# Kernel optimization log

Measured on AMD Instinct MI355X. Metric: run time of the kernel, lower is better.

The kernel has to match this reference:

```python
import jax, jax.numpy as jnp
import numpy as np
from jax import lax

TH = 1.0  # fire threshold (init kwarg th)


def setup_inputs() -> dict:
    key = jax.random.key(0)
    k0, k1, k2 = jax.random.split(key, 3)
    B, T, C = 32, 3000, 512
    hs_pad = jax.random.normal(k0, (B, T, C), dtype=jnp.float32)
    hs_mask = jnp.ones((B, 1, T), dtype=jnp.int32)  # espnet-style [B,1,T] mask, 1=valid
    # Conv1d(C, C, k=5) weight layout [out, in, k], fan-in scaled
    conv_w = jax.random.normal(k1, (C, C, 5), dtype=jnp.float32) * (1.0 / np.sqrt(C * 5))
    conv_b = jnp.zeros((C,), dtype=jnp.float32)
    # Linear(C, 1): stored transposed as [C, 1]
    lin_w = jax.random.normal(k2, (C, 1), dtype=jnp.float32) * (1.0 / np.sqrt(C))
    lin_b = jnp.zeros((1,), dtype=jnp.float32)
    return dict(hs_pad=hs_pad, hs_mask=hs_mask, conv_w=conv_w, conv_b=conv_b,
                lin_w=lin_w, lin_b=lin_b)


def _cif_single(alpha, h, th):
    """Integrate-and-fire for one sequence. alpha:[T], h:[T,C] -> [T,C] (zero padded)."""
    T, C = h.shape

    def step(carry, inp):
        acc, hacc = carry
        a, hu = inp
        acc2 = acc + a
        fired = acc2 >= th
        a1 = th - acc  # = th - (acc2 - a)
        emit = jnp.where(fired, hacc + a1 * hu, jnp.zeros_like(hu))
        new_acc = jnp.where(fired, a - a1, acc2)
        new_h = jnp.where(fired, (a - a1) * hu, hacc + a * hu)
        return (new_acc, new_h), (fired, emit)

    (acc_f, h_f), (fired, emits) = lax.scan(
        step, (jnp.float32(0.0), jnp.zeros((C,), h.dtype)), (alpha, h))
    nfire = jnp.cumsum(fired.astype(jnp.int32))
    idx = jnp.where(fired, nfire - 1, T)  # non-fired steps dump into scratch row T
    out = jnp.zeros((T + 1, C), h.dtype).at[idx].add(emits)
    # tail emission: remaining mass >= th/2
    tail = acc_f >= th * 0.5
    tail_idx = jnp.where(tail, nfire[-1], T)
    out = out.at[tail_idx].add(jnp.where(tail, h_f, jnp.zeros_like(h_f)))
    return out[:T]  # fires <= T always (alpha < 1 = th)


def _forward(hs_pad, hs_mask, conv_w, conv_b, lin_w, lin_b):
    B, T, C = hs_pad.shape
    # Conv1d(C,C,5,pad=2) on [B,C,T]  (note: self.norm is never used in the torch forward)
    x = lax.conv_general_dilated(hs_pad.transpose(0, 2, 1), conv_w, (1,), [(2, 2)],
                                 dimension_numbers=('NCH', 'OIH', 'NCH'))
    x = jax.nn.relu(x + conv_b[None, :, None])  # [B,C,T]
    alpha = jax.nn.sigmoid(jnp.einsum('bct,co->bto', x, lin_w) + lin_b)  # [B,T,1]
    # ys_pad=None -> T_y = 0; loss computed BEFORE masking (as in torch)
    loss_pen = jnp.abs(alpha.sum(axis=1) - 0.0).sum()
    a = alpha[..., 0] * (hs_mask[:, 0, :] != 0).astype(alpha.dtype)  # masked_fill(mask==0, 0)
    cs = jax.vmap(lambda av, hv: _cif_single(av, hv, TH))(a, hs_pad)  # [B,T,C]
    cs_mask = jnp.any(cs != 0.0, axis=-1)[:, None, :]  # [B,1,T]
    return cs, cs_mask, loss_pen


def reference(hs_pad, hs_mask, conv_w, conv_b, lin_w, lin_b):
    return _forward(hs_pad, hs_mask, conv_w, conv_b, lin_w, lin_b)
```

## Files before the change

### kernel.cpp

```cpp
#include <hip/hip_runtime.h>
#include <math.h>

#define B_ 32
#define T_ 3000
#define C_ 512
#define THf 1.0f
#define KW 2560

typedef _Float16 f16;
typedef _Float16 half8 __attribute__((ext_vector_type(8)));
typedef float floatx4 __attribute__((ext_vector_type(4)));

#define GLOBAL_AS __attribute__((address_space(1)))
#define LDS_AS __attribute__((address_space(3)))

#define WHI_OFF   0
#define WLO_OFF   2621440
#define PL_OFF    5242880
#define ALPHA_OFF 8314880
#define SEGI_OFF  8698880
#define SEGW_OFF  9466880
#define TOT_OFF   10234880

#define CS_SIZE  ((size_t)B_ * T_ * C_)
#define MASK_OFF CS_SIZE
#define LOSS_OFF (CS_SIZE + (size_t)B_ * T_)

__global__ __launch_bounds__(256) void w_prep_kernel(
    const float* __restrict__ W, f16* __restrict__ whi, f16* __restrict__ wlo)
{
    int idx = blockIdx.x * 256 + threadIdx.x;
    if (idx >= 512 * KW) return;
    int ie = idx & 7;
    int o  = (idx >> 3) & 511;
    int i8 = (idx >> 12) & 63;
    int k  = idx >> 18;
    int i  = i8 * 8 + ie;
    float w = W[o * KW + i * 5 + k];
    f16 h = (f16)w;
    whi[idx] = h;
    wlo[idx] = (f16)((w - (float)h) * 2048.0f);
}

#define A_ROWS 132
#define ALO_OFF_E  8448
#define WB_OFF_E   16896
#define WB_ARR_E   4096

__global__ __launch_bounds__(256, 2) void conv_alpha_mfma(
    const float* __restrict__ hs, const f16* __restrict__ whi_g,
    const f16* __restrict__ wlo_g, const float* __restrict__ conv_b,
    const float* __restrict__ lin_w, float* __restrict__ pl)
{
    __shared__ f16 sm[33280];
    f16* Ahi = sm;
    f16* Alo = sm + ALO_OFF_E;
    f16* Wb  = sm + WB_OFF_E;

    int tid = threadIdx.x;
    int bid = blockIdx.x;
    int nb  = bid & 3;
    int mtg = bid >> 2;
    int b   = mtg / 24;
    int mt  = mtg - b * 24;
    int t0  = mt * 128;

    int wid = tid >> 6, l = tid & 63;
    int wm = wid >> 1, wn = wid & 1;
    int l15 = l & 15, l4 = l >> 4;

    const float* hb = hs + (size_t)b * T_ * C_;
    int o0 = nb * 128;

    floatx4 acc1[4][4], acc2[4][4];
#pragma unroll
    for (int mf = 0; mf < 4; ++mf)
#pragma unroll
        for (int nf = 0; nf < 4; ++nf) {
            acc1[mf][nf] = (floatx4)0.f;
            acc2[mf][nf] = (floatx4)0.f;
        }

    auto issue_w = [&](int s2) {
        int buf = s2 & 1;
        int ic2 = s2 / 10, kk2 = s2 % 10;
        int k2 = kk2 >> 1, sub2 = kk2 & 1;
        int i8b = ic2 * 8 + sub2 * 4;
#pragma unroll
        for (int rr = 0; rr < 4; ++rr) {
            int r = wid * 4 + rr;
            int arr = r >> 3, kc = (r >> 1) & 3, oh = r & 1;
            const f16* gsrc = (arr ? wlo_g : whi_g) +
                ((size_t)((k2 * 64 + i8b + kc) * 512 + o0 + oh * 64 + l)) * 8;
            f16* ldst = Wb + (buf * 2 + arr) * WB_ARR_E + (kc * 128 + oh * 64) * 8;
            __builtin_amdgcn_global_load_lds((const GLOBAL_AS void*)gsrc,
                                             (LDS_AS void*)ldst, 16, 0, 0);
        }
    };

    issue_w(0);

    for (int s = 0; s < 80; ++s) {
        int ic = s / 10, kk = s % 10;
        int k = kk >> 1, sub = kk & 1;
        int buf = s & 1;

        if (kk == 0) {
            int i0 = ic * 64;
            for (int j = tid; j < A_ROWS * 8; j += 256) {
                int r = j >> 3, c = j & 7;
                int t = t0 - 2 + r;
                float4 v0 = make_float4(0.f, 0.f, 0.f, 0.f);
                float4 v1 = v0;
                if ((unsigned)t < (unsigned)T_) {
                    const float4* p = (const float4*)(hb + (size_t)t * C_ + i0 + c * 8);
                    v0 = p[0]; v1 = p[1];
                }
                float vv[8] = {v0.x, v0.y, v0.z, v0.w, v1.x, v1.y, v1.z, v1.w};
                half8 hh, ll;
#pragma unroll
                for (int q = 0; q < 8; ++q) {
                    f16 x = (f16)vv[q];
                    hh[q] = x;
                    ll[q] = (f16)((vv[q] - (float)x) * 2048.f);
                }
                int off = r * 64 + (c ^ (r & 7)) * 8;
                *(half8*)(Ahi + off) = hh;
                *(half8*)(Alo + off) = ll;
            }
            __syncthreads();
        }

        if (s + 1 < 80) issue_w(s + 1);

        half8 ah[4], al[4], bh[4], bl[4];
#pragma unroll
        for (int f = 0; f < 4; ++f) {
            int ar = wm * 64 + f * 16 + l15 + k;
            int aoff = ar * 64 + ((((sub << 2) | l4) ^ (ar & 7)) << 3);
            ah[f] = *(const half8*)(Ahi + aoff);
            al[f] = *(const half8*)(Alo + aoff);
            int wrow = l4 * 128 + wn * 64 + f * 16 + l15;
            bh[f] = *(const half8*)(Wb + (buf * 2 + 0) * WB_ARR_E + wrow * 8);
            bl[f] = *(const half8*)(Wb + (buf * 2 + 1) * WB_ARR_E + wrow * 8);
        }
        __builtin_amdgcn_s_setprio(1);
#pragma unroll
        for (int mf = 0; mf < 4; ++mf)
#pragma unroll
            for (int nf = 0; nf < 4; ++nf) {
                acc1[mf][nf] = __builtin_amdgcn_mfma_f32_16x16x32_f16(
                    ah[mf], bh[nf], acc1[mf][nf], 0, 0, 0);
                acc2[mf][nf] = __builtin_amdgcn_mfma_f32_16x16x32_f16(
                    al[mf], bh[nf], acc2[mf][nf], 0, 0, 0);
                acc2[mf][nf] = __builtin_amdgcn_mfma_f32_16x16x32_f16(
                    ah[mf], bl[nf], acc2[mf][nf], 0, 0, 0);
            }
        __builtin_amdgcn_s_setprio(0);
        __syncthreads();
    }

    float cb[4], lw[4];
#pragma unroll
    for (int nf = 0; nf < 4; ++nf) {
        int o = o0 + wn * 64 + nf * 16 + l15;
        cb[nf] = conv_b[o];
        lw[nf] = lin_w[o];
    }
    float* plb = pl + (size_t)(nb * 2 + wn) * (B_ * T_) + b * T_;
#pragma unroll
    for (int mf = 0; mf < 4; ++mf) {
#pragma unroll
        for (int reg = 0; reg < 4; ++reg) {
            float v = 0.f;
#pragma unroll
            for (int nf = 0; nf < 4; ++nf) {
                float c = acc1[mf][nf][reg] + acc2[mf][nf][reg] * (1.0f / 2048.0f);
                v += fmaxf(c + cb[nf], 0.f) * lw[nf];
            }
            v += __shfl_xor(v, 1);
            v += __shfl_xor(v, 2);
            v += __shfl_xor(v, 4);
            v += __shfl_xor(v, 8);
            int trow = t0 + wm * 64 + mf * 16 + l4 * 4 + reg;
            if (l15 == reg && trow < T_) plb[trow] = v;
        }
    }
}

__global__ __launch_bounds__(256) void alpha_combine_kernel(
    const float* __restrict__ pl, const float* __restrict__ lin_b,
    float* __restrict__ alpha)
{
    int idx = blockIdx.x * 256 + threadIdx.x;
    if (idx >= B_ * T_) return;
    float s = lin_b[0];
#pragma unroll
    for (int p = 0; p < 8; ++p) s += pl[(size_t)p * (B_ * T_) + idx];
    alpha[idx] = 1.f / (1.f + expf(-s));
}

__global__ __launch_bounds__(64) void scan_kernel(
    float* __restrict__ alpha, const int* __restrict__ mask,
    int2* __restrict__ seg_i, float2* __restrict__ seg_w,
    int* __restrict__ total_rows, float* __restrict__ out_loss)
{
    int lane = threadIdx.x;
    float lsum = 0.f;
    if (lane < B_) {
        const float4* ap = (const float4*)(alpha + lane * T_);
        const int4*   mp = (const int4*)(mask + lane * T_);
        float* astore = alpha + lane * T_;
        int2*   si = seg_i + lane * T_;
        float2* sw = seg_w + lane * T_;

        float acc = 0.f, leftover = 0.f;
        int nf = 0, prev_t = -1;

        float4 c0 = ap[0], c1 = ap[1];
        int4   m0 = mp[0], m1 = mp[1];
        for (int tc = 0; tc < T_ / 8; ++tc) {
            float4 n0, n1; int4 nm0, nm1;
            if (tc + 1 < T_ / 8) {
                n0 = ap[(tc + 1) * 2]; n1 = ap[(tc + 1) * 2 + 1];
                nm0 = mp[(tc + 1) * 2]; nm1 = mp[(tc + 1) * 2 + 1];
            }
            float av[8] = {c0.x, c0.y, c0.z, c0.w, c1.x, c1.y, c1.z, c1.w};
            int   mv[8] = {m0.x, m0.y, m0.z, m0.w, m1.x, m1.y, m1.z, m1.w};
#pragma unroll
            for (int u = 0; u < 8; ++u) {
                int t = tc * 8 + u;
                float araw = av[u];
                lsum += araw;
                float a = (mv[u] != 0) ? araw : 0.f;
                astore[t] = a;
                float acc2 = acc + a;
                float a1 = THf - acc;
                if (acc2 >= THf) {
                    si[nf] = make_int2(prev_t, t);
                    sw[nf] = make_float2(leftover, a1);
                    float rem = a - a1;
                    leftover = rem;
                    acc = rem;
                    prev_t = t;
                    ++nf;
                } else {
                    acc = acc2;
                }
            }
            c0 = n0; c1 = n1; m0 = nm0; m1 = nm1;
        }
        int tot = nf;
        if (acc >= 0.5f * THf) {
            si[nf] = make_int2(prev_t, T_);
            sw[nf] = make_float2(leftover, 0.f);
            ++tot;
        }
        total_rows[lane] = tot;
        lsum = fabsf(lsum);
    }
#pragma unroll
    for (int off = 16; off >= 1; off >>= 1) lsum += __shfl_down(lsum, off);
    if (lane == 0) out_loss[0] = lsum;
}

__global__ __launch_bounds__(128) void emit_kernel(
    const float* __restrict__ hs, const float* __restrict__ alpha,
    const int2* __restrict__ seg_i, const float2* __restrict__ seg_w,
    const int* __restrict__ total_rows, float* __restrict__ out)
{
    int blk = blockIdx.x;
    int b = blk / T_;
    int r = blk % T_;
    int tid = threadIdx.x;

    float4* cs4 = (float4*)(out + ((size_t)b * T_ + r) * C_);
    float* maskp = out + MASK_OFF + (size_t)b * T_ + r;
    int tot = total_rows[b];

    if (r >= tot) {
        float4 z; z.x = 0.f; z.y = 0.f; z.z = 0.f; z.w = 0.f;
        cs4[tid] = z;
        if (tid == 0) *maskp = 0.f;
        return;
    }
    int2   si = seg_i[b * T_ + r];
    float2 sw = seg_w[b * T_ + r];
    const float4* hb = (const float4*)(hs + (size_t)b * T_ * C_);
    const float*  ab = alpha + b * T_;

    float4 acc; acc.x = 0.f; acc.y = 0.f; acc.z = 0.f; acc.w = 0.f;
    int ts = si.x, te = si.y;
    if (ts >= 0) {
        float4 h = hb[(size_t)ts * (C_ / 4) + tid];
        acc.x = sw.x * h.x; acc.y = sw.x * h.y; acc.z = sw.x * h.z; acc.w = sw.x * h.w;
    }
    for (int t = ts + 1; t < te; ++t) {
        float a = ab[t];
        float4 h = hb[(size_t)t * (C_ / 4) + tid];
        acc.x = fmaf(a, h.x, acc.x); acc.y = fmaf(a, h.y, acc.y);
        acc.z = fmaf(a, h.z, acc.z); acc.w = fmaf(a, h.w, acc.w);
    }
    if (te < T_) {
        float4 h = hb[(size_t)te * (C_ / 4) + tid];
        acc.x = fmaf(sw.y, h.x, acc.x); acc.y = fmaf(sw.y, h.y, acc.y);
        acc.z = fmaf(sw.y, h.z, acc.z); acc.w = fmaf(sw.y, h.w, acc.w);
    }
    cs4[tid] = acc;
    if (tid == 0) *maskp = 1.f;
}

extern "C" void kernel_launch(void* const* d_in, const int* in_sizes, int n_in,
                              void* d_out, int out_size, void* d_ws, size_t ws_size,
                              hipStream_t stream)
{
    const float* hs     = (const float*)d_in[0];
    const int*   hmask  = (const int*)d_in[1];
    const float* conv_w = (const float*)d_in[2];
    const float* conv_b = (const float*)d_in[3];
    const float* lin_w  = (const float*)d_in[4];
    const float* lin_b  = (const float*)d_in[5];
    float* out = (float*)d_out;
    char*  ws  = (char*)d_ws;

    f16*    whi   = (f16*)(ws + WHI_OFF);
    f16*    wlo   = (f16*)(ws + WLO_OFF);
    float*  pl    = (float*)(ws + PL_OFF);
    float*  alpha = (float*)(ws + ALPHA_OFF);
    int2*   seg_i = (int2*)(ws + SEGI_OFF);
    float2* seg_w = (float2*)(ws + SEGW_OFF);
    int*    tot   = (int*)(ws + TOT_OFF);

    w_prep_kernel<<<(512 * KW + 255) / 256, 256, 0, stream>>>(conv_w, whi, wlo);
    conv_alpha_mfma<<<B_ * 24 * 4, 256, 0, stream>>>(hs, whi, wlo, conv_b, lin_w, pl);
    alpha_combine_kernel<<<(B_ * T_ + 255) / 256, 256, 0, stream>>>(pl, lin_b, alpha);
    scan_kernel<<<1, 64, 0, stream>>>(alpha, hmask, seg_i, seg_w, tot, out + LOSS_OFF);
    emit_kernel<<<B_ * T_, 128, 0, stream>>>(hs, alpha, seg_i, seg_w, tot, out);
}
```

Measured before the change: 971.3 us.

## Pre-split activations to swizzled fp16 hi/lo and stream them into LDS asynchronously

Adds a pre-pass that converts hs into a fp16 hi/lo split, stored per 32-channel chunk in a swizzled layout in workspace. A new conv kernel then loads A tiles with global_load_lds directly into double-buffered LDS, overlapping them with the MFMA loop instead of converting fp32 inside the GEMM. This costs an extra full pass over hs and roughly 200MB of workspace, so it only runs when the workspace is large enough; otherwise the old kernel path is kept.

```diff
diff --git a/kernel.cpp b/kernel.cpp
--- a/kernel.cpp
+++ b/kernel.cpp
@@ -14,17 +14,29 @@
 #define GLOBAL_AS __attribute__((address_space(1)))
 #define LDS_AS __attribute__((address_space(3)))
 
-#define WHI_OFF   0
-#define WLO_OFF   2621440
-#define PL_OFF    5242880
-#define ALPHA_OFF 8314880
-#define SEGI_OFF  8698880
-#define SEGW_OFF  9466880
-#define TOT_OFF   10234880
-
 #define CS_SIZE  ((size_t)B_ * T_ * C_)
 #define MASK_OFF CS_SIZE
 #define LOSS_OFF (CS_SIZE + (size_t)B_ * T_)
+
+#define HS16_ELEMS   ((size_t)B_ * 16 * 3000 * 64)
+#define HS16_ZEL     HS16_ELEMS
+#define HS16_BYTES   (2 * (HS16_ELEMS + 64))
+#define A_WHI_OFF    HS16_BYTES
+#define A_WLO_OFF    (A_WHI_OFF + 2621440)
+#define A_PL_OFF     (A_WLO_OFF + 2621440)
+#define A_ALPHA_OFF  (A_PL_OFF + 3072000)
+#define A_SEGI_OFF   (A_ALPHA_OFF + 384000)
+#define A_SEGW_OFF   (A_SEGI_OFF + 768000)
+#define A_TOT_OFF    (A_SEGW_OFF + 768000)
+#define A_WS_NEED    (A_TOT_OFF + 128)
+
+#define B_WHI_OFF   0
+#define B_WLO_OFF   2621440
+#define B_PL_OFF    5242880
+#define B_ALPHA_OFF 8314880
+#define B_SEGI_OFF  8698880
+#define B_SEGW_OFF  9466880
+#define B_TOT_OFF   10234880
 
 __global__ __launch_bounds__(256) void w_prep_kernel(
     const float* __restrict__ W, f16* __restrict__ whi, f16* __restrict__ wlo)
@@ -42,12 +54,162 @@
     wlo[idx] = (f16)((w - (float)h) * 2048.0f);
 }
 
+__global__ __launch_bounds__(256) void hs_split_kernel(
+    const float* __restrict__ hs, f16* __restrict__ hs16)
+{
+    size_t idx = (size_t)blockIdx.x * 256 + threadIdx.x;
+    if (idx < 64) hs16[HS16_ZEL + idx] = (f16)0.f;
+    if (idx >= (size_t)B_ * 16 * 3000 * 32) return;
+    int ie  = idx & 31;
+    size_t row = idx >> 5;
+    int t   = (int)(row % 3000);
+    int bic = (int)(row / 3000);
+    int b   = bic >> 4;
+    int ic  = bic & 15;
+    float v = hs[((size_t)b * 3000 + t) * 512 + ic * 32 + ie];
+    f16 h = (f16)v;
+    f16 l = (f16)((v - (float)h) * 2048.0f);
+    int m7 = (t + 2) & 7;
+    size_t rb = row * 64;
+    int ch = (ie >> 3), e = ie & 7;
+    hs16[rb + (size_t)((ch ^ m7) * 8 + e)] = h;
+    hs16[rb + (size_t)(((ch + 4) ^ m7) * 8 + e)] = l;
+}
+
+__global__ __launch_bounds__(256, 2) void conv_alpha_mfma_a(
+    const f16* __restrict__ hs16, const f16* __restrict__ whi_g,
+    const f16* __restrict__ wlo_g, const float* __restrict__ conv_b,
+    const float* __restrict__ lin_w, float* __restrict__ pl)
+{
+    __shared__ f16 sm[33792];
+
+    int tid = threadIdx.x;
+    int bid = blockIdx.x;
+    int nb  = bid & 3;
+    int mtg = bid >> 2;
+    int b   = mtg / 24;
+    int mt  = mtg - b * 24;
+    int t0  = mt * 128;
+
+    int wid = tid >> 6, l = tid & 63;
+    int wm = wid >> 1, wn = wid & 1;
+    int l15 = l & 15, l4 = l >> 4;
+    int o0 = nb * 128;
+
+    floatx4 acc1[4][4], acc2[4][4];
+#pragma unroll
+    for (int mf = 0; mf < 4; ++mf)
+#pragma unroll
+        for (int nf = 0; nf < 4; ++nf) {
+            acc1[mf][nf] = (floatx4)0.f;
+            acc2[mf][nf] = (floatx4)0.f;
+        }
+
+    auto issue_a = [&](int icn) {
+        const f16* hbase = hs16 + ((size_t)(b * 16 + icn)) * 3000 * 64;
+        f16* abase = sm + (icn & 1) * 8704;
+        for (int j = wid; j < 17; j += 4) {
+            int r = j * 8 + (l >> 3);
+            int t = t0 - 2 + r;
+            const f16* gsrc = ((unsigned)t < 3000u)
+                ? hbase + (size_t)t * 64 + (l & 7) * 8
+                : hs16 + HS16_ZEL + (l & 7) * 8;
+            __builtin_amdgcn_global_load_lds((const GLOBAL_AS void*)gsrc,
+                                             (LDS_AS void*)(abase + j * 512), 16, 0, 0);
+        }
+    };
+    auto issue_w = [&](int s2) {
+        int buf = s2 & 1;
+        int ic2 = s2 / 5, k2 = s2 - ic2 * 5;
+#pragma unroll
+        for (int rr = 0; rr < 4; ++rr) {
+            int r = wid * 4 + rr;
+            int arr = r >> 3, kc = (r >> 1) & 3, oh = r & 1;
+            const f16* gsrc = (arr ? wlo_g : whi_g) +
+                ((size_t)((k2 * 64 + ic2 * 4 + kc) * 512 + o0 + oh * 64 + l)) * 8;
+            f16* ldst = sm + 17408 + (buf * 2 + arr) * 4096 + (kc * 128 + oh * 64) * 8;
+            __builtin_amdgcn_global_load_lds((const GLOBAL_AS void*)gsrc,
+                                             (LDS_AS void*)ldst, 16, 0, 0);
+        }
+    };
+
+    issue_a(0);
+    issue_w(0);
+    __syncthreads();
+
+    for (int s = 0; s < 80; ++s) {
+        int ic = s / 5, k = s - ic * 5;
+        int abuf = ic & 1, wbuf = s & 1;
+        if (k == 0 && ic + 1 < 16) issue_a(ic + 1);
+        if (s + 1 < 80) issue_w(s + 1);
+
+        const f16* Ab = sm + abuf * 8704;
+        const f16* Wh = sm + 17408 + (wbuf * 2 + 0) * 4096;
+        const f16* Wl = sm + 17408 + (wbuf * 2 + 1) * 4096;
+        int m7 = (l15 + k) & 7;
+        int sh = (l4 ^ m7) * 8;
+        int sl = ((l4 + 4) ^ m7) * 8;
+
+        half8 ah[4], al[4], bh[4], bl[4];
+#pragma unroll
+        for (int f = 0; f < 4; ++f) {
+            int r = wm * 64 + f * 16 + l15 + k;
+            ah[f] = *(const half8*)(Ab + r * 64 + sh);
+            al[f] = *(const half8*)(Ab + r * 64 + sl);
+            int wrow = l4 * 128 + wn * 64 + f * 16 + l15;
+            bh[f] = *(const half8*)(Wh + wrow * 8);
+            bl[f] = *(const half8*)(Wl + wrow * 8);
+        }
+        __builtin_amdgcn_s_setprio(1);
+#pragma unroll
+        for (int mf = 0; mf < 4; ++mf)
+#pragma unroll
+            for (int nf = 0; nf < 4; ++nf) {
+                acc1[mf][nf] = __builtin_amdgcn_mfma_f32_16x16x32_f16(
+                    ah[mf], bh[nf], acc1[mf][nf], 0, 0, 0);
+                acc2[mf][nf] = __builtin_amdgcn_mfma_f32_16x16x32_f16(
+                    al[mf], bh[nf], acc2[mf][nf], 0, 0, 0);
+                acc2[mf][nf] = __builtin_amdgcn_mfma_f32_16x16x32_f16(
+                    ah[mf], bl[nf], acc2[mf][nf], 0, 0, 0);
+            }
+        __builtin_amdgcn_s_setprio(0);
+        __syncthreads();
+    }
+
+    float cb[4], lw[4];
+#pragma unroll
+    for (int nf = 0; nf < 4; ++nf) {
+        int o = o0 + wn * 64 + nf * 16 + l15;
+        cb[nf] = conv_b[o];
+        lw[nf] = lin_w[o];
+    }
+    float* plb = pl + (size_t)(nb * 2 + wn) * (B_ * T_) + b * T_;
+#pragma unroll
+    for (int mf = 0; mf < 4; ++mf) {
+#pragma unroll
+        for (int reg = 0; reg < 4; ++reg) {
+            float v = 0.f;
+#pragma unroll
+            for (int nf = 0; nf < 4; ++nf) {
+                float c = acc1[mf][nf][reg] + acc2[mf][nf][reg] * (1.0f / 2048.0f);
+                v += fmaxf(c + cb[nf], 0.f) * lw[nf];
+            }
+            v += __shfl_xor(v, 1);
+            v += __shfl_xor(v, 2);
+            v += __shfl_xor(v, 4);
+            v += __shfl_xor(v, 8);
+            int trow = t0 + wm * 64 + mf * 16 + l4 * 4 + reg;
+            if (l15 == reg && trow < T_) plb[trow] = v;
+        }
+    }
+}
+
 #define A_ROWS 132
 #define ALO_OFF_E  8448
 #define WB_OFF_E   16896
 #define WB_ARR_E   4096
 
-__global__ __launch_bounds__(256, 2) void conv_alpha_mfma(
+__global__ __launch_bounds__(256, 2) void conv_alpha_mfma_b(
     const float* __restrict__ hs, const f16* __restrict__ whi_g,
     const f16* __restrict__ wlo_g, const float* __restrict__ conv_b,
     const float* __restrict__ lin_w, float* __restrict__ pl)
@@ -323,17 +485,38 @@
     float* out = (float*)d_out;
     char*  ws  = (char*)d_ws;
 
-    f16*    whi   = (f16*)(ws + WHI_OFF);
-    f16*    wlo   = (f16*)(ws + WLO_OFF);
-    float*  pl    = (float*)(ws + PL_OFF);
-    float*  alpha = (float*)(ws + ALPHA_OFF);
-    int2*   seg_i = (int2*)(ws + SEGI_OFF);
-    float2* seg_w = (float2*)(ws + SEGW_OFF);
-    int*    tot   = (int*)(ws + TOT_OFF);
-
-    w_prep_kernel<<<(512 * KW + 255) / 256, 256, 0, stream>>>(conv_w, whi, wlo);
-    conv_alpha_mfma<<<B_ * 24 * 4, 256, 0, stream>>>(hs, whi, wlo, conv_b, lin_w, pl);
-    alpha_combine_kernel<<<(B_ * T_ + 255) / 256, 256, 0, stream>>>(pl, lin_b, alpha);
-    scan_kernel<<<1, 64, 0, stream>>>(alpha, hmask, seg_i, seg_w, tot, out + LOSS_OFF);
-    emit_kernel<<<B_ * T_, 128, 0, stream>>>(hs, alpha, seg_i, seg_w, tot, out);
-}
+    if (ws_size >= (size_t)A_WS_NEED) {
+        f16*    hs16  = (f16*)ws;
+        f16*    whi   = (f16*)(ws + A_WHI_OFF);
+        f16*    wlo   = (f16*)(ws + A_WLO_OFF);
+        float*  pl    = (float*)(ws + A_PL_OFF);
+        float*  alpha = (float*)(ws + A_ALPHA_OFF);
+        int2*   seg_i = (int2*)(ws + A_SEGI_OFF);
+        float2* seg_w = (float2*)(ws + A_SEGW_OFF);
+        int*    tot   = (int*)(ws + A_TOT_OFF);
+
+        w_prep_kernel<<<(512 * KW + 255) / 256, 256, 0, stream>>>(conv_w, whi, wlo);
+        hs_split_kernel<<<(int)(((size_t)B_ * 16 * 3000 * 32 + 255) / 256), 256, 0,
+                          stream>>>(hs, hs16);
+        conv_alpha_mfma_a<<<B_ * 24 * 4, 256, 0, stream>>>(hs16, whi, wlo, conv_b,
+                                                           lin_w, pl);
+        alpha_combine_kernel<<<(B_ * T_ + 255) / 256, 256, 0, stream>>>(pl, lin_b, alpha);
+        scan_kernel<<<1, 64, 0, stream>>>(alpha, hmask, seg_i, seg_w, tot, out + LOSS_OFF);
+        emit_kernel<<<B_ * T_, 128, 0, stream>>>(hs, alpha, seg_i, seg_w, tot, out);
+    } else {
+        f16*    whi   = (f16*)(ws + B_WHI_OFF);
+        f16*    wlo   = (f16*)(ws + B_WLO_OFF);
+        float*  pl    = (float*)(ws + B_PL_OFF);
+        float*  alpha = (float*)(ws + B_ALPHA_OFF);
+        int2*   seg_i = (int2*)(ws + B_SEGI_OFF);
+        float2* seg_w = (float2*)(ws + B_SEGW_OFF);
+        int*    tot   = (int*)(ws + B_TOT_OFF);
+
+        w_prep_kernel<<<(512 * KW + 255) / 256, 256, 0, stream>>>(conv_w, whi, wlo);
+        conv_alpha_mfma_b<<<B_ * 24 * 4, 256, 0, stream>>>(hs, whi, wlo, conv_b,
+                                                           lin_w, pl);
+        alpha_combine_kernel<<<(B_ * T_ + 255) / 256, 256, 0, stream>>>(pl, lin_b, alpha);
+        scan_kernel<<<1, 64, 0, stream>>>(alpha, hmask, seg_i, seg_w, tot, out + LOSS_OFF);
+        emit_kernel<<<B_ * T_, 128, 0, stream>>>(hs, alpha, seg_i, seg_w, tot, out);
+    }
+}
```

Measured after the change: 1.047 ms. 7.8% more time.

## Restructure conv MFMA kernel with register-staged A pipeline and direct weight loads

Applied to the files above, without the earlier changes.

Rewrites the conv-alpha kernel so that activations are prefetched into registers and written into a double-buffered LDS tile in 32-channel chunks. Weights are now loaded from global memory straight into registers with ping-pong prefetch, replacing the LDS staging path. Both products go into a single accumulator by pre-scaling the low parts with 1/64 in fp16, which removes the second accumulator set. It also remaps block IDs for better cache locality. The changes cut LDS traffic, accumulator registers and barriers, but risk extra global-load latency and some precision loss from the smaller low-part scale and fp16 pre-scaling.

```diff
diff --git a/kernel.cpp b/kernel.cpp
--- a/kernel.cpp
+++ b/kernel.cpp
@@ -13,6 +13,12 @@
 
 #define GLOBAL_AS __attribute__((address_space(1)))
 #define LDS_AS __attribute__((address_space(3)))
+
+#define CS_SIZE  ((size_t)B_ * T_ * C_)
+#define MASK_OFF CS_SIZE
+#define LOSS_OFF (CS_SIZE + (size_t)B_ * T_)
+
+#define LOSC 64.0f
 
 #define WHI_OFF   0
 #define WLO_OFF   2621440
@@ -21,10 +27,6 @@
 #define SEGI_OFF  8698880
 #define SEGW_OFF  9466880
 #define TOT_OFF   10234880
-
-#define CS_SIZE  ((size_t)B_ * T_ * C_)
-#define MASK_OFF CS_SIZE
-#define LOSS_OFF (CS_SIZE + (size_t)B_ * T_)
 
 __global__ __launch_bounds__(256) void w_prep_kernel(
     const float* __restrict__ W, f16* __restrict__ whi, f16* __restrict__ wlo)
@@ -39,26 +41,19 @@
     float w = W[o * KW + i * 5 + k];
     f16 h = (f16)w;
     whi[idx] = h;
-    wlo[idx] = (f16)((w - (float)h) * 2048.0f);
-}
-
-#define A_ROWS 132
-#define ALO_OFF_E  8448
-#define WB_OFF_E   16896
-#define WB_ARR_E   4096
-
-__global__ __launch_bounds__(256, 2) void conv_alpha_mfma(
+    wlo[idx] = (f16)((w - (float)h) * LOSC);
+}
+
+__global__ __launch_bounds__(256, 2) void conv_alpha_mfma_a(
     const float* __restrict__ hs, const f16* __restrict__ whi_g,
     const f16* __restrict__ wlo_g, const float* __restrict__ conv_b,
     const float* __restrict__ lin_w, float* __restrict__ pl)
 {
-    __shared__ f16 sm[33280];
-    f16* Ahi = sm;
-    f16* Alo = sm + ALO_OFF_E;
-    f16* Wb  = sm + WB_OFF_E;
-
-    int tid = threadIdx.x;
-    int bid = blockIdx.x;
+    __shared__ f16 sm[2][8704];
+
+    int tid  = threadIdx.x;
+    int orig = blockIdx.x;
+    int bid  = (orig & 7) * 384 + (orig >> 3);
     int nb  = bid & 3;
     int mtg = bid >> 2;
     int b   = mtg / 24;
@@ -68,97 +63,138 @@
     int wid = tid >> 6, l = tid & 63;
     int wm = wid >> 1, wn = wid & 1;
     int l15 = l & 15, l4 = l >> 4;
+    int o0 = nb * 128;
 
     const float* hb = hs + (size_t)b * T_ * C_;
-    int o0 = nb * 128;
-
-    floatx4 acc1[4][4], acc2[4][4];
+
+    floatx4 acc[4][4];
 #pragma unroll
     for (int mf = 0; mf < 4; ++mf)
 #pragma unroll
-        for (int nf = 0; nf < 4; ++nf) {
-            acc1[mf][nf] = (floatx4)0.f;
-            acc2[mf][nf] = (floatx4)0.f;
-        }
-
-    auto issue_w = [&](int s2) {
-        int buf = s2 & 1;
-        int ic2 = s2 / 10, kk2 = s2 % 10;
-        int k2 = kk2 >> 1, sub2 = kk2 & 1;
-        int i8b = ic2 * 8 + sub2 * 4;
-#pragma unroll
-        for (int rr = 0; rr < 4; ++rr) {
-            int r = wid * 4 + rr;
-            int arr = r >> 3, kc = (r >> 1) & 3, oh = r & 1;
-            const f16* gsrc = (arr ? wlo_g : whi_g) +
-                ((size_t)((k2 * 64 + i8b + kc) * 512 + o0 + oh * 64 + l)) * 8;
-            f16* ldst = Wb + (buf * 2 + arr) * WB_ARR_E + (kc * 128 + oh * 64) * 8;
-            __builtin_amdgcn_global_load_lds((const GLOBAL_AS void*)gsrc,
-                                             (LDS_AS void*)ldst, 16, 0, 0);
+        for (int nf = 0; nf < 4; ++nf) acc[mf][nf] = (floatx4)0.f;
+
+    float4 sA[3][2];
+    auto stage_load = [&](int icn) {
+#pragma unroll
+        for (int u = 0; u < 3; ++u) {
+            int j = tid + u * 256;
+            float4 z = make_float4(0.f, 0.f, 0.f, 0.f);
+            sA[u][0] = z; sA[u][1] = z;
+            if (j < 544) {
+                int r = j >> 2, c = j & 3;
+                int t = t0 - 2 + r;
+                if ((unsigned)t < 3000u) {
+                    const float4* p =
+                        (const float4*)(hb + (size_t)t * C_ + icn * 32 + c * 8);
+                    sA[u][0] = p[0];
+                    sA[u][1] = p[1];
+                }
+            }
         }
     };
-
-    issue_w(0);
-
-    for (int s = 0; s < 80; ++s) {
-        int ic = s / 10, kk = s % 10;
-        int k = kk >> 1, sub = kk & 1;
-        int buf = s & 1;
-
-        if (kk == 0) {
-            int i0 = ic * 64;
-            for (int j = tid; j < A_ROWS * 8; j += 256) {
-                int r = j >> 3, c = j & 7;
-                int t = t0 - 2 + r;
-                float4 v0 = make_float4(0.f, 0.f, 0.f, 0.f);
-                float4 v1 = v0;
-                if ((unsigned)t < (unsigned)T_) {
-                    const float4* p = (const float4*)(hb + (size_t)t * C_ + i0 + c * 8);
-                    v0 = p[0]; v1 = p[1];
-                }
-                float vv[8] = {v0.x, v0.y, v0.z, v0.w, v1.x, v1.y, v1.z, v1.w};
+    auto stage_write = [&](int abuf) {
+#pragma unroll
+        for (int u = 0; u < 3; ++u) {
+            int j = tid + u * 256;
+            if (j < 544) {
+                int r = j >> 2, c = j & 3;
+                float vv[8] = {sA[u][0].x, sA[u][0].y, sA[u][0].z, sA[u][0].w,
+                               sA[u][1].x, sA[u][1].y, sA[u][1].z, sA[u][1].w};
                 half8 hh, ll;
 #pragma unroll
                 for (int q = 0; q < 8; ++q) {
                     f16 x = (f16)vv[q];
                     hh[q] = x;
-                    ll[q] = (f16)((vv[q] - (float)x) * 2048.f);
+                    ll[q] = (f16)((vv[q] - (float)x) * LOSC);
                 }
-                int off = r * 64 + (c ^ (r & 7)) * 8;
-                *(half8*)(Ahi + off) = hh;
-                *(half8*)(Alo + off) = ll;
-            }
-            __syncthreads();
-        }
-
-        if (s + 1 < 80) issue_w(s + 1);
-
-        half8 ah[4], al[4], bh[4], bl[4];
-#pragma unroll
-        for (int f = 0; f < 4; ++f) {
-            int ar = wm * 64 + f * 16 + l15 + k;
-            int aoff = ar * 64 + ((((sub << 2) | l4) ^ (ar & 7)) << 3);
-            ah[f] = *(const half8*)(Ahi + aoff);
-            al[f] = *(const half8*)(Alo + aoff);
-            int wrow = l4 * 128 + wn * 64 + f * 16 + l15;
-            bh[f] = *(const half8*)(Wb + (buf * 2 + 0) * WB_ARR_E + wrow * 8);
-            bl[f] = *(const half8*)(Wb + (buf * 2 + 1) * WB_ARR_E + wrow * 8);
-        }
-        __builtin_amdgcn_s_setprio(1);
-#pragma unroll
-        for (int mf = 0; mf < 4; ++mf)
-#pragma unroll
-            for (int nf = 0; nf < 4; ++nf) {
-                acc1[mf][nf] = __builtin_amdgcn_mfma_f32_16x16x32_f16(
-                    ah[mf], bh[nf], acc1[mf][nf], 0, 0, 0);
-                acc2[mf][nf] = __builtin_amdgcn_mfma_f32_16x16x32_f16(
-                    al[mf], bh[nf], acc2[mf][nf], 0, 0, 0);
-                acc2[mf][nf] = __builtin_amdgcn_mfma_f32_16x16x32_f16(
-                    ah[mf], bl[nf], acc2[mf][nf], 0, 0, 0);
-            }
-        __builtin_amdgcn_s_setprio(0);
-        __syncthreads();
-    }
+                f16* base = &sm[abuf][0] + r * 64;
+                int swz = r & 7;
+                *(half8*)(base + (((c)     ^ swz) << 3)) = hh;
+                *(half8*)(base + (((c + 4) ^ swz) << 3)) = ll;
+            }
+        }
+    };
+
+    const f16* whiL = whi_g + ((l4 * 512) + o0 + wn * 64 + l15) * 8;
+    const f16* wloL = wlo_g + ((l4 * 512) + o0 + wn * 64 + l15) * 8;
+
+    const f16 inv64 = (f16)0.015625f;
+
+    half8 bhA[4], blA[4], bhB[4], blB[4];
+
+    stage_load(0);
+#pragma unroll
+    for (int nf = 0; nf < 4; ++nf) {
+        bhA[nf] = *(const half8*)(whiL + nf * 128);
+        blA[nf] = *(const half8*)(wloL + nf * 128);
+    }
+    stage_write(0);
+    __syncthreads();
+
+#define CONV_STEP(KK, BHC, BLC, BHN, BLN)                                     \
+    do {                                                                      \
+        const int kk_ = (KK);                                                 \
+        const int kcur_ = kk_ % 5;                                            \
+        const int bufc_ = (kk_ < 5) ? 0 : 1;                                  \
+        if (kk_ == 0) stage_load(icB);                                        \
+        if (kk_ == 3) stage_write(1);                                         \
+        if (kk_ == 5) stage_load((icA + 2 <= 15) ? icA + 2 : 15);             \
+        if (kk_ == 8) stage_write(0);                                         \
+        {                                                                     \
+            int nic_ = (kk_ + 1 < 5) ? icA                                    \
+                       : ((kk_ + 1 < 10) ? icB                                \
+                                         : ((icA + 2 <= 15) ? icA + 2 : 15)); \
+            int nk_ = (kk_ + 1) % 5;                                          \
+            int st_ = (nk_ * 64 + nic_ * 4) * 4096;                           \
+            _Pragma("unroll")                                                 \
+            for (int nf = 0; nf < 4; ++nf) {                                  \
+                BHN[nf] = *(const half8*)(whiL + st_ + nf * 128);             \
+                BLN[nf] = *(const half8*)(wloL + st_ + nf * 128);             \
+            }                                                                 \
+        }                                                                     \
+        {                                                                     \
+            const f16* Ab_ = &sm[bufc_][0];                                   \
+            int m7_ = (l15 + kcur_) & 7;                                      \
+            int sh_ = (l4 ^ m7_) * 8;                                         \
+            int sl_ = ((l4 + 4) ^ m7_) * 8;                                   \
+            __builtin_amdgcn_s_setprio(1);                                    \
+            _Pragma("unroll")                                                 \
+            for (int mf = 0; mf < 4; ++mf) {                                  \
+                int r_ = wm * 64 + mf * 16 + l15 + kcur_;                     \
+                half8 ah = *(const half8*)(Ab_ + r_ * 64 + sh_);              \
+                half8 al = *(const half8*)(Ab_ + r_ * 64 + sl_);              \
+                half8 ahd = ah * inv64;                                       \
+                half8 ald = al * inv64;                                       \
+                _Pragma("unroll")                                             \
+                for (int nf = 0; nf < 4; ++nf) {                              \
+                    acc[mf][nf] = __builtin_amdgcn_mfma_f32_16x16x32_f16(     \
+                        ah, BHC[nf], acc[mf][nf], 0, 0, 0);                   \
+                    acc[mf][nf] = __builtin_amdgcn_mfma_f32_16x16x32_f16(     \
+                        ald, BHC[nf], acc[mf][nf], 0, 0, 0);                  \
+                    acc[mf][nf] = __builtin_amdgcn_mfma_f32_16x16x32_f16(     \
+                        ahd, BLC[nf], acc[mf][nf], 0, 0, 0);                  \
+                }                                                             \
+            }                                                                 \
+            __builtin_amdgcn_s_setprio(0);                                    \
+        }                                                                     \
+        if (kk_ == 4 || kk_ == 9) __syncthreads();                            \
+    } while (0)
+
+    for (int ic2 = 0; ic2 < 8; ++ic2) {
+        int icA = ic2 * 2;
+        int icB = icA + 1;
+        CONV_STEP(0, bhA, blA, bhB, blB);
+        CONV_STEP(1, bhB, blB, bhA, blA);
+        CONV_STEP(2, bhA, blA, bhB, blB);
+        CONV_STEP(3, bhB, blB, bhA, blA);
+        CONV_STEP(4, bhA, blA, bhB, blB);
+        CONV_STEP(5, bhB, blB, bhA, blA);
+        CONV_STEP(6, bhA, blA, bhB, blB);
+        CONV_STEP(7, bhB, blB, bhA, blA);
+        CONV_STEP(8, bhA, blA, bhB, blB);
+        CONV_STEP(9, bhB, blB, bhA, blA);
+    }
+#undef CONV_STEP
 
     float cb[4], lw[4];
 #pragma unroll
@@ -175,7 +211,7 @@
             float v = 0.f;
 #pragma unroll
             for (int nf = 0; nf < 4; ++nf) {
-                float c = acc1[mf][nf][reg] + acc2[mf][nf][reg] * (1.0f / 2048.0f);
+                float c = acc[mf][nf][reg];
                 v += fmaxf(c + cb[nf], 0.f) * lw[nf];
             }
             v += __shfl_xor(v, 1);
@@ -332,7 +368,8 @@
     int*    tot   = (int*)(ws + TOT_OFF);
 
     w_prep_kernel<<<(512 * KW + 255) / 256, 256, 0, stream>>>(conv_w, whi, wlo);
-    conv_alpha_mfma<<<B_ * 24 * 4, 256, 0, stream>>>(hs, whi, wlo, conv_b, lin_w, pl);
+    conv_alpha_mfma_a<<<B_ * 24 * 4, 256, 0, stream>>>(hs, whi, wlo, conv_b,
+                                                       lin_w, pl);
     alpha_combine_kernel<<<(B_ * T_ + 255) / 256, 256, 0, stream>>>(pl, lin_b, alpha);
     scan_kernel<<<1, 64, 0, stream>>>(alpha, hmask, seg_i, seg_w, tot, out + LOSS_OFF);
     emit_kernel<<<B_ * T_, 128, 0, stream>>>(hs, alpha, seg_i, seg_w, tot, out);
```

Measured after the change: 943.5 us, median of 4. 2.9% less time.
